# Kernel tuning notes

Measured on AMD Instinct MI355X. Metric: run time of the kernel, lower is better.

Reference implementation:

```python
import jax, jax.numpy as jnp
import numpy as np

N, E, C, NB = 10000, 160000, 32, 8  # atoms, edges, channels, radial basis


def _W(k, shp):
    return jax.random.normal(k, shp, jnp.float32) / np.float32(np.sqrt(shp[0]))


def setup_inputs():
    ks = jax.random.split(jax.random.key(0), 16)
    return {
        "p1": jax.random.normal(ks[0], (N, C), jnp.float32),
        "p3": jax.random.normal(ks[1], (N, 3, C), jnp.float32),
        "r3": jax.random.normal(ks[2], (E, 3), jnp.float32),
        "basis": jax.random.normal(ks[3], (E, NB), jnp.float32),
        "idx_i": jax.random.randint(ks[4], (E,), 0, N, jnp.int32),
        "idx_j": jax.random.randint(ks[5], (E,), 0, N, jnp.int32),
        "pp1_W": _W(ks[6], (C, C)), "pp1_b": jnp.zeros((C,), jnp.float32),
        "pi1_W1": _W(ks[7], (2 * C, C)), "pi1_b1": jnp.zeros((C,), jnp.float32),
        "pi1_W2": _W(ks[8], (C, 3 * C)), "pi1_b2": jnp.zeros((3 * C,), jnp.float32),
        "pi1_W3": _W(ks[9], (3 * C, 3 * C * NB)),
        "ii1_W": _W(ks[10], (C, C)), "ii1_b": jnp.zeros((C,), jnp.float32),
        "pp3_W": _W(ks[11], (C, C)), "pp3_b": jnp.zeros((C,), jnp.float32),
        "pi3_W1": _W(ks[12], (2 * C, C)), "pi3_b1": jnp.zeros((C,), jnp.float32),
        "pi3_W2": _W(ks[13], (C, C)), "pi3_b2": jnp.zeros((C,), jnp.float32),
        "pi3_W3": _W(ks[14], (C, C * NB)),
        "ii3_W": _W(ks[15], (C, C)), "ii3_b": jnp.zeros((C,), jnp.float32),
    }


def _pi_layer(prop, idx_i, idx_j, basis, W1, b1, W2, b2, W3, out_c):
    # gather both endpoints, concat, linear MLP (no activation, no last bias),
    # contract trailing basis axis with per-edge basis functions
    inter = jnp.concatenate([prop[idx_i], prop[idx_j]], axis=-1)  # [E, ..., 2C]
    h = inter @ W1 + b1
    h = h @ W2 + b2
    h = h @ W3                                   # [E, ..., out_c*NB]
    h = h.reshape(h.shape[:-1] + (out_c, NB))
    return jnp.einsum('e...cb,eb->e...c', h, basis)


def _forward(p1, p3, r3, basis, idx_i, idx_j,
             pp1_W, pp1_b, pi1_W1, pi1_b1, pi1_W2, pi1_b2, pi1_W3, ii1_W, ii1_b,
             pp3_W, pp3_b, pi3_W1, pi3_b1, pi3_W2, pi3_b2, pi3_W3, ii3_W, ii3_b):
    act = jnp.tanh
    # rank-1 branch
    p1h = act(p1 @ pp1_W + pp1_b)                                   # [N, C]
    i1 = _pi_layer(p1h, idx_i, idx_j, basis,
                   pi1_W1, pi1_b1, pi1_W2, pi1_b2, pi1_W3, 3 * C)   # [E, 3C]
    i1_1, i1_2, i1_3 = jnp.split(i1, 3, axis=-1)
    i1a = act(i1_1 @ ii1_W + ii1_b)                                  # [E, C]
    p1n = jax.ops.segment_sum(i1a, idx_j, num_segments=N)            # [N, C]
    # rank-3 (vector) branch
    p3h = act(p3 @ pp3_W + pp3_b)                                    # [N, 3, C]
    i3 = _pi_layer(p3h, idx_i, idx_j, basis,
                   pi3_W1, pi3_b1, pi3_W2, pi3_b2, pi3_W3, C)        # [E, 3, C]
    i3 = act(i3 @ ii3_W + ii3_b)
    # equivariant scale/add: i3*i1_2 + r3*i1_3 (broadcast over Cartesian axis)
    i3 = i3 * i1_2[:, None, :] + r3[:, :, None] * i1_3[:, None, :]   # [E, 3, C]
    p3n = jax.ops.segment_sum(i3, idx_j, num_segments=N)             # [N, 3, C]
    # dot layer + residual into p1, then rescale p3 by p1
    p1o = jnp.sum(p3n * p3n, axis=1) + p1n                           # [N, C]
    p3o = p3n * p1o[:, None, :]                                      # [N, 3, C]
    return p1o, p3o


def reference(p1, p3, r3, basis, idx_i, idx_j,
              pp1_W, pp1_b, pi1_W1, pi1_b1, pi1_W2, pi1_b2, pi1_W3, ii1_W, ii1_b,
              pp3_W, pp3_b, pi3_W1, pi3_b1, pi3_W2, pi3_b2, pi3_W3, ii3_W, ii3_b):
    return _forward(p1, p3, r3, basis, idx_i, idx_j,
                    pp1_W, pp1_b, pi1_W1, pi1_b1, pi1_W2, pi1_b2, pi1_W3, ii1_W, ii1_b,
                    pp3_W, pp3_b, pi3_W1, pi3_b1, pi3_W2, pi3_b2, pi3_W3, ii3_W, ii3_b)
```

## Files before the change

kernel.cpp:

```cpp
#include <hip/hip_runtime.h>
#include <math.h>

#define NN 10000
#define NE 160000

typedef __attribute__((ext_vector_type(8))) short s8v;
typedef __attribute__((ext_vector_type(4))) float f4v;
typedef unsigned short u16;

#define OFF_P1HB 0u
#define OFF_P3HB 640000u
#define OFF_WB   2560000u
#define OFF_P1N  2736640u
#define OFF_P3N  4016640u

#define OWF1  0
#define OBB1  49152
#define OII1T 52224
#define OWF3  53248
#define OBB3  69632
#define OII3T 70656
#define NWB   71680

__device__ __forceinline__ short f2b(float f) {
    unsigned u = __float_as_uint(f);
    u += 0x7fffu + ((u >> 16) & 1u);
    return (short)(u >> 16);
}
__device__ __forceinline__ float tanhf_fast(float x) {
    float xc = fminf(9.f, fmaxf(-9.f, x));
    float e = __expf(2.f * xc);
    return (e - 1.f) * __builtin_amdgcn_rcpf(e + 1.f);
}

__global__ __launch_bounds__(256) void prep_kernel(
    const float* __restrict__ p1, const float* __restrict__ p3,
    const float* __restrict__ pp1_W, const float* __restrict__ pp1_b,
    const float* __restrict__ pp3_W, const float* __restrict__ pp3_b,
    const float* __restrict__ W1, const float* __restrict__ W2,
    const float* __restrict__ W3,
    const float* __restrict__ b1v, const float* __restrict__ b2v,
    const float* __restrict__ ii1,
    const float* __restrict__ W13, const float* __restrict__ W23,
    const float* __restrict__ W33,
    const float* __restrict__ b13v, const float* __restrict__ b23v,
    const float* __restrict__ ii3,
    u16* __restrict__ p1hb, u16* __restrict__ p3hb,
    u16* __restrict__ wb, float* __restrict__ p1n)
{
    __shared__ float smem[6912];
    const int blk = blockIdx.x;
    const int tid = threadIdx.x;

    if (blk < 64) {
        const int cb0 = blk * 12;
        float* sW1  = smem;
        float* sW2  = smem + 2048;
        float* sW3c = smem + 5120;
        float* sU   = smem + 6272;
        float* sbt  = smem + 6656;
        for (int i = tid; i < 2048; i += 256) sW1[i] = W1[i];
        for (int i = tid; i < 3072; i += 256) sW2[i] = W2[i];
        for (int i = tid; i < 1152; i += 256) {
            int q = i / 12, u = i % 12;
            sW3c[i] = W3[q * 768 + cb0 + u];
        }
        __syncthreads();
        for (int t = tid; t < 480; t += 256) {
            if (t < 384) {
                int c2 = t / 12, u = t % 12;
                float a = 0.f;
                #pragma unroll 8
                for (int q = 0; q < 96; ++q) a += sW2[c2 * 96 + q] * sW3c[q * 12 + u];
                sU[t] = a;
            } else {
                int q = t - 384;
                float a = b2v[q];
                #pragma unroll 8
                for (int c2 = 0; c2 < 32; ++c2) a += b1v[c2] * sW2[c2 * 96 + q];
                sbt[q] = a;
            }
        }
        __syncthreads();
        for (int o = tid; o < 768; o += 256) {
            int k = o / 12, u = o % 12;
            float a = 0.f;
            #pragma unroll 8
            for (int c2 = 0; c2 < 32; ++c2) a += sW1[k * 32 + c2] * sU[c2 * 12 + u];
            int cb = cb0 + u, b = cb & 7, c = cb >> 3;
            int nt = c >> 4, cL = c & 15;
            int ks = k >> 5, k5 = k & 31, Lhi = k5 >> 3, j = k5 & 7;
            wb[OWF1 + b * 6144 + nt * 1024 + ks * 512 + (Lhi * 16 + cL) * 8 + j] = (u16)f2b(a);
        }
        for (int o = tid; o < 48; o += 256) {
            int u = o >> 2, Lhi = o & 3;
            int x = cb0 + u;
            float a = 0.f;
            if (Lhi == 0) {
                #pragma unroll 8
                for (int q = 0; q < 96; ++q) a += sbt[q] * sW3c[q * 12 + u];
            }
            int j = x & 7, c = x >> 3, nt = c >> 4, cL = c & 15;
            wb[OBB1 + nt * 512 + (Lhi * 16 + cL) * 8 + j] = (u16)f2b(a);
        }
    } else if (blk < 96) {
        const int cb0 = (blk - 64) * 8;
        float* sW13  = smem;
        float* sW23  = smem + 2048;
        float* sW33c = smem + 3072;
        float* sU3   = smem + 3328;
        float* sbt3  = smem + 3584;
        for (int i = tid; i < 2048; i += 256) sW13[i] = W13[i];
        for (int i = tid; i < 1024; i += 256) sW23[i] = W23[i];
        for (int i = tid; i < 256; i += 256) {
            int q = i / 8, u = i % 8;
            sW33c[i] = W33[q * 256 + cb0 + u];
        }
        __syncthreads();
        for (int t = tid; t < 288; t += 256) {
            if (t < 256) {
                int c2 = t / 8, u = t % 8;
                float a = 0.f;
                #pragma unroll 8
                for (int q = 0; q < 32; ++q) a += sW23[c2 * 32 + q] * sW33c[q * 8 + u];
                sU3[t] = a;
            } else {
                int q = t - 256;
                float a = b23v[q];
                #pragma unroll 8
                for (int c2 = 0; c2 < 32; ++c2) a += b13v[c2] * sW23[c2 * 32 + q];
                sbt3[q] = a;
            }
        }
        __syncthreads();
        for (int o = tid; o < 512; o += 256) {
            int k = o / 8, u = o % 8;
            float a = 0.f;
            #pragma unroll 8
            for (int c2 = 0; c2 < 32; ++c2) a += sW13[k * 32 + c2] * sU3[c2 * 8 + u];
            int cb = cb0 + u, b = cb & 7, c = cb >> 3;
            int nt = c >> 4, cL = c & 15;
            int ks = k >> 5, k5 = k & 31, Lhi = k5 >> 3, j = k5 & 7;
            wb[OWF3 + b * 2048 + nt * 1024 + ks * 512 + (Lhi * 16 + cL) * 8 + j] = (u16)f2b(a);
        }
        for (int o = tid; o < 32; o += 256) {
            int u = o >> 2, Lhi = o & 3;
            int x = cb0 + u;
            float a = 0.f;
            if (Lhi == 0) {
                #pragma unroll
                for (int q = 0; q < 32; ++q) a += sbt3[q] * sW33c[q * 8 + u];
            }
            int j = x & 7, c = x >> 3, nt = c >> 4, cL = c & 15;
            wb[OBB3 + nt * 512 + (Lhi * 16 + cL) * 8 + j] = (u16)f2b(a);
        }
    } else if (blk == 96) {
        for (int i = tid; i < 2048; i += 256) {
            if (i < 1024) {
                int nt = i >> 9, L = (i >> 3) & 63, j = i & 7;
                wb[OII1T + i] = (u16)f2b(ii1[((L >> 4) * 8 + j) * 32 + 16 * nt + (L & 15)]);
            } else {
                int i2 = i - 1024;
                int nt = i2 >> 9, L = (i2 >> 3) & 63, j = i2 & 7;
                wb[OII3T + i2] = (u16)f2b(ii3[((L >> 4) * 8 + j) * 32 + 16 * nt + (L & 15)]);
            }
        }
    } else if (blk < 5097) {
        float* Ws0 = smem;
        float* Ws1 = smem + 1024;
        float* bs0 = smem + 2048;
        float* bs1 = smem + 2080;
        for (int i = tid; i < 1024; i += 256) { Ws0[i] = pp1_W[i]; Ws1[i] = pp3_W[i]; }
        if (tid < 32) { bs0[tid] = pp1_b[tid]; bs1[tid] = pp3_b[tid]; }
        __syncthreads();
        int idx = (blk - 97) * 256 + tid;
        int n = idx >> 7;
        int r = (idx >> 5) & 3;
        int c = idx & 31;
        const float* Ws = (r == 0) ? Ws0 : Ws1;
        const float* bs = (r == 0) ? bs0 : bs1;
        const float* in = (r == 0) ? (p1 + n * 32) : (p3 + (n * 3 + (r - 1)) * 32);
        float acc = bs[c];
        #pragma unroll
        for (int k = 0; k < 32; ++k) acc += in[k] * Ws[k * 32 + c];
        short v = f2b(tanhf(acc));
        if (r == 0) p1hb[n * 32 + c] = (u16)v;
        else        p3hb[(n * 3 + (r - 1)) * 32 + c] = (u16)v;
    } else {
        float4 z = make_float4(0.f, 0.f, 0.f, 0.f);
        ((float4*)p1n)[(size_t)(blk - 5097) * 256 + tid] = z;
    }
}

__global__ __launch_bounds__(64, 3) void edge_kernel(
    const u16* __restrict__ p1hb, const u16* __restrict__ p3hb,
    const float* __restrict__ r3, const float* __restrict__ basis,
    const int* __restrict__ idx_i, const int* __restrict__ idx_j,
    const u16* __restrict__ wb,
    const float* __restrict__ ii1b, const float* __restrict__ ii3b,
    float* __restrict__ p1n, float* __restrict__ p3n)
{
    __shared__ int4 smem4[136];
    char* sw = (char*)smem4;
    int*   sIdxI = (int*)(sw + 0);
    int*   sIdxJ = (int*)(sw + 64);
    float* sBasT = (float*)(sw + 128);
    float* sR3   = (float*)(sw + 640);
    u16*   sT2   = (u16*)(sw + 832);

    const int l   = threadIdx.x & 63;
    const int r16 = l & 15;
    const int kg  = l >> 4;
    const int ebase = blockIdx.x * 16;

    if (l < 16)      sIdxI[l] = idx_i[ebase + l];
    else if (l < 32) sIdxJ[l - 16] = idx_j[ebase + l - 16];
    else if (l < 48) {
        int e = l - 32;
        sR3[e]      = r3[(size_t)(ebase + e) * 3 + 0];
        sR3[16 + e] = r3[(size_t)(ebase + e) * 3 + 1];
        sR3[32 + e] = r3[(size_t)(ebase + e) * 3 + 2];
    }
    if (l < 32) {
        int e = l >> 1, hf = l & 1;
        float4 q = ((const float4*)(basis + (size_t)(ebase + e) * 8))[hf];
        sBasT[(4 * hf + 0) * 16 + e] = q.x;
        sBasT[(4 * hf + 1) * 16 + e] = q.y;
        sBasT[(4 * hf + 2) * 16 + e] = q.z;
        sBasT[(4 * hf + 3) * 16 + e] = q.w;
    }

    const float vii1[2] = { ii1b[r16], ii1b[16 + r16] };
    const float vii3[2] = { ii3b[r16], ii3b[16 + r16] };

    const f4v zf = {0.f, 0.f, 0.f, 0.f};

    s8v bA;
    {
        s8v t;
        #pragma unroll
        for (int j = 0; j < 8; ++j)
            t[j] = (kg == 0) ? f2b(sBasT[j * 16 + r16]) : (short)0;
        bA = t;
    }

    s8v avI = *(const s8v*)(p1hb + (size_t)sIdxI[r16] * 32 + kg * 8);
    s8v avJ = *(const s8v*)(p1hb + (size_t)sIdxJ[r16] * 32 + kg * 8);

    f4v accT[6];
    {
        const u16* gBB = wb + OBB1;
        #pragma unroll
        for (int nt = 0; nt < 6; ++nt) {
            s8v bbv = *(const s8v*)(gBB + (nt * 64 + l) * 8);
            accT[nt] = __builtin_amdgcn_mfma_f32_16x16x32_bf16(bA, bbv, zf, 0, 0, 0);
        }
    }

    {
        const u16* gW = wb + OWF1;
        #pragma unroll 2
        for (int b = 0; b < 8; ++b) {
            float tb[4];
            #pragma unroll
            for (int rr = 0; rr < 4; ++rr)
                tb[rr] = sBasT[b * 16 + 4 * kg + rr];
            #pragma unroll
            for (int nt = 0; nt < 6; ++nt) {
                const u16* bp = gW + ((size_t)(b * 6 + nt) * 2) * 512 + l * 8;
                s8v bv0 = *(const s8v*)(bp);
                s8v bv1 = *(const s8v*)(bp + 512);
                f4v D = __builtin_amdgcn_mfma_f32_16x16x32_bf16(avI, bv0, zf, 0, 0, 0);
                D = __builtin_amdgcn_mfma_f32_16x16x32_bf16(avJ, bv1, D, 0, 0, 0);
                #pragma unroll
                for (int rr = 0; rr < 4; ++rr)
                    accT[nt][rr] += tb[rr] * D[rr];
            }
        }
    }

    {
        const u16* gII = wb + OII1T;
        #pragma unroll
        for (int nt = 0; nt < 2; ++nt)
            #pragma unroll
            for (int rr = 0; rr < 4; ++rr)
                sT2[(4 * kg + rr) * 40 + 16 * nt + r16] = (u16)f2b(accT[nt][rr]);
        s8v av = *(const s8v*)(sT2 + r16 * 40 + 8 * kg);
        #pragma unroll
        for (int nt = 0; nt < 2; ++nt) {
            s8v bv = *(const s8v*)(gII + (nt * 64 + l) * 8);
            f4v ia = __builtin_amdgcn_mfma_f32_16x16x32_bf16(av, bv, zf, 0, 0, 0);
            #pragma unroll
            for (int rr = 0; rr < 4; ++rr) {
                int rowD = 4 * kg + rr;
                atomicAdd(&p1n[(size_t)sIdxJ[rowD] * 32 + 16 * nt + r16],
                          tanhf_fast(ia[rr] + vii1[nt]));
            }
        }
    }

    const u16* gW3  = wb + OWF3;
    const u16* gBB3 = wb + OBB3;
    const u16* gII3 = wb + OII3T;
    for (int d = 0; d < 3; ++d) {
        s8v avI3 = *(const s8v*)(p3hb + ((size_t)sIdxI[r16] * 3 + d) * 32 + kg * 8);
        s8v avJ3 = *(const s8v*)(p3hb + ((size_t)sIdxJ[r16] * 3 + d) * 32 + kg * 8);
        f4v accP[2];
        #pragma unroll
        for (int nt = 0; nt < 2; ++nt) {
            s8v bbv = *(const s8v*)(gBB3 + (nt * 64 + l) * 8);
            accP[nt] = __builtin_amdgcn_mfma_f32_16x16x32_bf16(bA, bbv, zf, 0, 0, 0);
        }
        #pragma unroll 2
        for (int b = 0; b < 8; ++b) {
            float tb[4];
            #pragma unroll
            for (int rr = 0; rr < 4; ++rr)
                tb[rr] = sBasT[b * 16 + 4 * kg + rr];
            #pragma unroll
            for (int nt = 0; nt < 2; ++nt) {
                const u16* bp = gW3 + ((size_t)(b * 2 + nt) * 2) * 512 + l * 8;
                s8v bv0 = *(const s8v*)(bp);
                s8v bv1 = *(const s8v*)(bp + 512);
                f4v D = __builtin_amdgcn_mfma_f32_16x16x32_bf16(avI3, bv0, zf, 0, 0, 0);
                D = __builtin_amdgcn_mfma_f32_16x16x32_bf16(avJ3, bv1, D, 0, 0, 0);
                #pragma unroll
                for (int rr = 0; rr < 4; ++rr)
                    accP[nt][rr] += tb[rr] * D[rr];
            }
        }
        #pragma unroll
        for (int nt = 0; nt < 2; ++nt)
            #pragma unroll
            for (int rr = 0; rr < 4; ++rr)
                sT2[(4 * kg + rr) * 40 + 16 * nt + r16] = (u16)f2b(accP[nt][rr]);
        s8v av = *(const s8v*)(sT2 + r16 * 40 + 8 * kg);
        #pragma unroll
        for (int nt = 0; nt < 2; ++nt) {
            s8v bv = *(const s8v*)(gII3 + (nt * 64 + l) * 8);
            f4v ja = __builtin_amdgcn_mfma_f32_16x16x32_bf16(av, bv, zf, 0, 0, 0);
            #pragma unroll
            for (int rr = 0; rr < 4; ++rr) {
                int rowD = 4 * kg + rr;
                float i3a = tanhf_fast(ja[rr] + vii3[nt]);
                float val = i3a * accT[2 + nt][rr] + sR3[d * 16 + rowD] * accT[4 + nt][rr];
                atomicAdd(&p3n[((size_t)sIdxJ[rowD] * 3 + d) * 32 + 16 * nt + r16], val);
            }
        }
    }
}

__global__ __launch_bounds__(256) void finalize_kernel(
    const float* __restrict__ p1n, const float* __restrict__ p3n,
    float* __restrict__ out)
{
    int t = blockIdx.x * 256 + threadIdx.x;
    int n = t >> 5, c = t & 31;
    float a0 = p3n[(n * 3 + 0) * 32 + c];
    float a1 = p3n[(n * 3 + 1) * 32 + c];
    float a2 = p3n[(n * 3 + 2) * 32 + c];
    float p1o = p1n[t] + a0 * a0 + a1 * a1 + a2 * a2;
    out[t] = p1o;
    float* o3 = out + NN * 32;
    o3[(n * 3 + 0) * 32 + c] = a0 * p1o;
    o3[(n * 3 + 1) * 32 + c] = a1 * p1o;
    o3[(n * 3 + 2) * 32 + c] = a2 * p1o;
}

extern "C" void kernel_launch(void* const* d_in, const int* in_sizes, int n_in,
                              void* d_out, int out_size, void* d_ws, size_t ws_size,
                              hipStream_t stream) {
    const float* p1     = (const float*)d_in[0];
    const float* p3     = (const float*)d_in[1];
    const float* r3     = (const float*)d_in[2];
    const float* basis  = (const float*)d_in[3];
    const int*   idx_i  = (const int*)d_in[4];
    const int*   idx_j  = (const int*)d_in[5];
    const float* pp1_W  = (const float*)d_in[6];
    const float* pp1_b  = (const float*)d_in[7];
    const float* pi1_W1 = (const float*)d_in[8];
    const float* pi1_b1 = (const float*)d_in[9];
    const float* pi1_W2 = (const float*)d_in[10];
    const float* pi1_b2 = (const float*)d_in[11];
    const float* pi1_W3 = (const float*)d_in[12];
    const float* ii1_W  = (const float*)d_in[13];
    const float* ii1_b  = (const float*)d_in[14];
    const float* pp3_W  = (const float*)d_in[15];
    const float* pp3_b  = (const float*)d_in[16];
    const float* pi3_W1 = (const float*)d_in[17];
    const float* pi3_b1 = (const float*)d_in[18];
    const float* pi3_W2 = (const float*)d_in[19];
    const float* pi3_b2 = (const float*)d_in[20];
    const float* pi3_W3 = (const float*)d_in[21];
    const float* ii3_W  = (const float*)d_in[22];
    const float* ii3_b  = (const float*)d_in[23];

    char* ws = (char*)d_ws;
    u16*   p1hb = (u16*)(ws + OFF_P1HB);
    u16*   p3hb = (u16*)(ws + OFF_P3HB);
    u16*   wb   = (u16*)(ws + OFF_WB);
    float* p1n  = (float*)(ws + OFF_P1N);
    float* p3n  = (float*)(ws + OFF_P3N);

    prep_kernel<<<dim3(6347), dim3(256), 0, stream>>>(
        p1, p3, pp1_W, pp1_b, pp3_W, pp3_b,
        pi1_W1, pi1_W2, pi1_W3, pi1_b1, pi1_b2, ii1_W,
        pi3_W1, pi3_W2, pi3_W3, pi3_b1, pi3_b2, ii3_W,
        p1hb, p3hb, wb, p1n);

    edge_kernel<<<dim3(NE / 16), dim3(64), 0, stream>>>(
        p1hb, p3hb, r3, basis, idx_i, idx_j, wb,
        ii1_b, ii3_b, p1n, p3n);

    finalize_kernel<<<dim3(1250), dim3(256), 0, stream>>>(p1n, p3n, (float*)d_out);
}
```

Before: 125.4 us.

## Replace atomic scatter with counting-sort ranks and per-node gather reduction

```diff
diff --git a/kernel.cpp b/kernel.cpp
--- a/kernel.cpp
+++ b/kernel.cpp
@@ -8,11 +8,14 @@
 typedef __attribute__((ext_vector_type(4))) float f4v;
 typedef unsigned short u16;
 
-#define OFF_P1HB 0u
-#define OFF_P3HB 640000u
-#define OFF_WB   2560000u
-#define OFF_P1N  2736640u
-#define OFF_P3N  4016640u
+#define OFF_P1HB  0u
+#define OFF_P3HB  640000u
+#define OFF_WB    2560000u
+#define OFF_HIST  2703360u
+#define OFF_CURSOR 2743360u
+#define OFF_START 2783360u
+#define OFF_RANK  2823364u
+#define OFF_E13   3463376u
 
 #define OWF1  0
 #define OBB1  49152
@@ -26,6 +29,9 @@
     unsigned u = __float_as_uint(f);
     u += 0x7fffu + ((u >> 16) & 1u);
     return (short)(u >> 16);
+}
+__device__ __forceinline__ float b2f(u16 s) {
+    return __uint_as_float(((unsigned)s) << 16);
 }
 __device__ __forceinline__ float tanhf_fast(float x) {
     float xc = fminf(9.f, fmaxf(-9.f, x));
@@ -45,8 +51,9 @@
     const float* __restrict__ W33,
     const float* __restrict__ b13v, const float* __restrict__ b23v,
     const float* __restrict__ ii3,
+    const int* __restrict__ idx_j,
     u16* __restrict__ p1hb, u16* __restrict__ p3hb,
-    u16* __restrict__ wb, float* __restrict__ p1n)
+    u16* __restrict__ wb, int* __restrict__ hist)
 {
     __shared__ float smem[6912];
     const int blk = blockIdx.x;
@@ -187,18 +194,52 @@
         if (r == 0) p1hb[n * 32 + c] = (u16)v;
         else        p3hb[(n * 3 + (r - 1)) * 32 + c] = (u16)v;
     } else {
-        float4 z = make_float4(0.f, 0.f, 0.f, 0.f);
-        ((float4*)p1n)[(size_t)(blk - 5097) * 256 + tid] = z;
-    }
+        int e = (blk - 5097) * 256 + tid;
+        if (e < NE) atomicAdd(&hist[idx_j[e]], 1);
+    }
+}
+
+__global__ __launch_bounds__(256) void scan_kernel(
+    const int* __restrict__ hist, int* __restrict__ start, int* __restrict__ cursor)
+{
+    __shared__ int part[256];
+    int t = threadIdx.x;
+    int base = t * 40;
+    int s = 0;
+    for (int i = 0; i < 40; ++i) { int idx = base + i; if (idx < NN) s += hist[idx]; }
+    part[t] = s;
+    __syncthreads();
+    for (int off = 1; off < 256; off <<= 1) {
+        int v = (t >= off) ? part[t - off] : 0;
+        __syncthreads();
+        part[t] += v;
+        __syncthreads();
+    }
+    int run = part[t] - s;
+    for (int i = 0; i < 40; ++i) {
+        int idx = base + i;
+        if (idx < NN) {
+            int h = hist[idx];
+            start[idx] = run; cursor[idx] = run; run += h;
+        }
+    }
+    if (t == 255) start[NN] = part[255];
+}
+
+__global__ __launch_bounds__(256) void rank_kernel(
+    const int* __restrict__ idx_j, int* __restrict__ cursor, int* __restrict__ rank)
+{
+    int e = blockIdx.x * 256 + threadIdx.x;
+    if (e < NE) rank[e] = atomicAdd(&cursor[idx_j[e]], 1);
 }
 
 __global__ __launch_bounds__(64, 3) void edge_kernel(
     const u16* __restrict__ p1hb, const u16* __restrict__ p3hb,
     const float* __restrict__ r3, const float* __restrict__ basis,
     const int* __restrict__ idx_i, const int* __restrict__ idx_j,
-    const u16* __restrict__ wb,
+    const int* __restrict__ rank, const u16* __restrict__ wb,
     const float* __restrict__ ii1b, const float* __restrict__ ii3b,
-    float* __restrict__ p1n, float* __restrict__ p3n)
+    u16* __restrict__ e13)
 {
     __shared__ int4 smem4[136];
     char* sw = (char*)smem4;
@@ -206,7 +247,8 @@
     int*   sIdxJ = (int*)(sw + 64);
     float* sBasT = (float*)(sw + 128);
     float* sR3   = (float*)(sw + 640);
-    u16*   sT2   = (u16*)(sw + 832);
+    int*   sRank = (int*)(sw + 832);
+    u16*   sT2   = (u16*)(sw + 896);
 
     const int l   = threadIdx.x & 63;
     const int r16 = l & 15;
@@ -220,6 +262,8 @@
         sR3[e]      = r3[(size_t)(ebase + e) * 3 + 0];
         sR3[16 + e] = r3[(size_t)(ebase + e) * 3 + 1];
         sR3[32 + e] = r3[(size_t)(ebase + e) * 3 + 2];
+    } else {
+        sRank[l - 48] = rank[ebase + l - 48];
     }
     if (l < 32) {
         int e = l >> 1, hf = l & 1;
@@ -287,16 +331,16 @@
             for (int rr = 0; rr < 4; ++rr)
                 sT2[(4 * kg + rr) * 40 + 16 * nt + r16] = (u16)f2b(accT[nt][rr]);
         s8v av = *(const s8v*)(sT2 + r16 * 40 + 8 * kg);
-        #pragma unroll
-        for (int nt = 0; nt < 2; ++nt) {
-            s8v bv = *(const s8v*)(gII + (nt * 64 + l) * 8);
-            f4v ia = __builtin_amdgcn_mfma_f32_16x16x32_bf16(av, bv, zf, 0, 0, 0);
-            #pragma unroll
-            for (int rr = 0; rr < 4; ++rr) {
-                int rowD = 4 * kg + rr;
-                atomicAdd(&p1n[(size_t)sIdxJ[rowD] * 32 + 16 * nt + r16],
-                          tanhf_fast(ia[rr] + vii1[nt]));
-            }
+        s8v bvA = *(const s8v*)(gII + (0 * 64 + l) * 8);
+        s8v bvB = *(const s8v*)(gII + (1 * 64 + l) * 8);
+        f4v ia0 = __builtin_amdgcn_mfma_f32_16x16x32_bf16(av, bvA, zf, 0, 0, 0);
+        f4v ia1 = __builtin_amdgcn_mfma_f32_16x16x32_bf16(av, bvB, zf, 0, 0, 0);
+        #pragma unroll
+        for (int rr = 0; rr < 4; ++rr) {
+            int rowD = 4 * kg + rr;
+            size_t base = (size_t)sRank[rowD] * 128;
+            e13[base + r16]      = (u16)f2b(tanhf_fast(ia0[rr] + vii1[0]));
+            e13[base + 16 + r16] = (u16)f2b(tanhf_fast(ia1[rr] + vii1[1]));
         }
     }
 
@@ -336,36 +380,62 @@
             for (int rr = 0; rr < 4; ++rr)
                 sT2[(4 * kg + rr) * 40 + 16 * nt + r16] = (u16)f2b(accP[nt][rr]);
         s8v av = *(const s8v*)(sT2 + r16 * 40 + 8 * kg);
-        #pragma unroll
-        for (int nt = 0; nt < 2; ++nt) {
-            s8v bv = *(const s8v*)(gII3 + (nt * 64 + l) * 8);
-            f4v ja = __builtin_amdgcn_mfma_f32_16x16x32_bf16(av, bv, zf, 0, 0, 0);
-            #pragma unroll
-            for (int rr = 0; rr < 4; ++rr) {
-                int rowD = 4 * kg + rr;
-                float i3a = tanhf_fast(ja[rr] + vii3[nt]);
-                float val = i3a * accT[2 + nt][rr] + sR3[d * 16 + rowD] * accT[4 + nt][rr];
-                atomicAdd(&p3n[((size_t)sIdxJ[rowD] * 3 + d) * 32 + 16 * nt + r16], val);
-            }
-        }
-    }
-}
-
-__global__ __launch_bounds__(256) void finalize_kernel(
-    const float* __restrict__ p1n, const float* __restrict__ p3n,
+        s8v bvA = *(const s8v*)(gII3 + (0 * 64 + l) * 8);
+        s8v bvB = *(const s8v*)(gII3 + (1 * 64 + l) * 8);
+        f4v ja0 = __builtin_amdgcn_mfma_f32_16x16x32_bf16(av, bvA, zf, 0, 0, 0);
+        f4v ja1 = __builtin_amdgcn_mfma_f32_16x16x32_bf16(av, bvB, zf, 0, 0, 0);
+        #pragma unroll
+        for (int rr = 0; rr < 4; ++rr) {
+            int rowD = 4 * kg + rr;
+            float rv = sR3[d * 16 + rowD];
+            float v0 = tanhf_fast(ja0[rr] + vii3[0]) * accT[2][rr] + rv * accT[4][rr];
+            float v1 = tanhf_fast(ja1[rr] + vii3[1]) * accT[3][rr] + rv * accT[5][rr];
+            size_t base = (size_t)sRank[rowD] * 128 + 32 + 32 * d;
+            e13[base + r16]      = (u16)f2b(v0);
+            e13[base + 16 + r16] = (u16)f2b(v1);
+        }
+    }
+}
+
+__global__ __launch_bounds__(256) void gather2(
+    const u16* __restrict__ e13, const int* __restrict__ start,
     float* __restrict__ out)
 {
-    int t = blockIdx.x * 256 + threadIdx.x;
-    int n = t >> 5, c = t & 31;
-    float a0 = p3n[(n * 3 + 0) * 32 + c];
-    float a1 = p3n[(n * 3 + 1) * 32 + c];
-    float a2 = p3n[(n * 3 + 2) * 32 + c];
-    float p1o = p1n[t] + a0 * a0 + a1 * a1 + a2 * a2;
-    out[t] = p1o;
-    float* o3 = out + NN * 32;
-    o3[(n * 3 + 0) * 32 + c] = a0 * p1o;
-    o3[(n * 3 + 1) * 32 + c] = a1 * p1o;
-    o3[(n * 3 + 2) * 32 + c] = a2 * p1o;
+    int node = blockIdx.x * 4 + (threadIdx.x >> 6);
+    int l = threadIdx.x & 63;
+    int st = start[node], en = start[node + 1];
+    int deg = en - st;
+    float a0 = 0.f, a1 = 0.f;
+    const u16* base = e13 + (size_t)st * 128 + 2 * l;
+    int k = 0;
+    for (; k + 4 <= deg; k += 4) {
+        unsigned v0 = *(const unsigned*)(base + (size_t)(k + 0) * 128);
+        unsigned v1 = *(const unsigned*)(base + (size_t)(k + 1) * 128);
+        unsigned v2 = *(const unsigned*)(base + (size_t)(k + 2) * 128);
+        unsigned v3 = *(const unsigned*)(base + (size_t)(k + 3) * 128);
+        a0 += b2f((u16)(v0 & 0xffffu)) + b2f((u16)(v1 & 0xffffu))
+            + b2f((u16)(v2 & 0xffffu)) + b2f((u16)(v3 & 0xffffu));
+        a1 += b2f((u16)(v0 >> 16)) + b2f((u16)(v1 >> 16))
+            + b2f((u16)(v2 >> 16)) + b2f((u16)(v3 >> 16));
+    }
+    for (; k < deg; ++k) {
+        unsigned v = *(const unsigned*)(base + (size_t)k * 128);
+        a0 += b2f((u16)(v & 0xffffu));
+        a1 += b2f((u16)(v >> 16));
+    }
+    int q = l & 15, g = l >> 4;
+    float s00 = __shfl(a0, q),      s10 = __shfl(a1, q);
+    float s01 = __shfl(a0, 16 + q), s11 = __shfl(a1, 16 + q);
+    float s02 = __shfl(a0, 32 + q), s12 = __shfl(a1, 32 + q);
+    float s03 = __shfl(a0, 48 + q), s13 = __shfl(a1, 48 + q);
+    float p1o0 = s00 + s01 * s01 + s02 * s02 + s03 * s03;
+    float p1o1 = s10 + s11 * s11 + s12 * s12 + s13 * s13;
+    if (g == 0) {
+        *(float2*)(out + (size_t)node * 32 + 2 * q) = make_float2(p1o0, p1o1);
+    } else {
+        float2 v = make_float2(a0 * p1o0, a1 * p1o1);
+        *(float2*)(out + (size_t)NN * 32 + ((size_t)node * 3 + (g - 1)) * 32 + 2 * q) = v;
+    }
 }
 
 extern "C" void kernel_launch(void* const* d_in, const int* in_sizes, int n_in,
@@ -397,21 +467,29 @@
     const float* ii3_b  = (const float*)d_in[23];
 
     char* ws = (char*)d_ws;
-    u16*   p1hb = (u16*)(ws + OFF_P1HB);
-    u16*   p3hb = (u16*)(ws + OFF_P3HB);
-    u16*   wb   = (u16*)(ws + OFF_WB);
-    float* p1n  = (float*)(ws + OFF_P1N);
-    float* p3n  = (float*)(ws + OFF_P3N);
-
-    prep_kernel<<<dim3(6347), dim3(256), 0, stream>>>(
+    u16* p1hb   = (u16*)(ws + OFF_P1HB);
+    u16* p3hb   = (u16*)(ws + OFF_P3HB);
+    u16* wb     = (u16*)(ws + OFF_WB);
+    int* hist   = (int*)(ws + OFF_HIST);
+    int* cursor = (int*)(ws + OFF_CURSOR);
+    int* startA = (int*)(ws + OFF_START);
+    int* rank   = (int*)(ws + OFF_RANK);
+    u16* e13    = (u16*)(ws + OFF_E13);
+
+    hipMemsetAsync(hist, 0, NN * sizeof(int), stream);
+
+    prep_kernel<<<dim3(5722), dim3(256), 0, stream>>>(
         p1, p3, pp1_W, pp1_b, pp3_W, pp3_b,
         pi1_W1, pi1_W2, pi1_W3, pi1_b1, pi1_b2, ii1_W,
         pi3_W1, pi3_W2, pi3_W3, pi3_b1, pi3_b2, ii3_W,
-        p1hb, p3hb, wb, p1n);
+        idx_j, p1hb, p3hb, wb, hist);
+
+    scan_kernel<<<dim3(1), dim3(256), 0, stream>>>(hist, startA, cursor);
+    rank_kernel<<<dim3((NE + 255) / 256), dim3(256), 0, stream>>>(idx_j, cursor, rank);
 
     edge_kernel<<<dim3(NE / 16), dim3(64), 0, stream>>>(
-        p1hb, p3hb, r3, basis, idx_i, idx_j, wb,
-        ii1_b, ii3_b, p1n, p3n);
-
-    finalize_kernel<<<dim3(1250), dim3(256), 0, stream>>>(p1n, p3n, (float*)d_out);
-}
+        p1hb, p3hb, r3, basis, idx_i, idx_j, rank, wb,
+        ii1_b, ii3_b, e13);
+
+    gather2<<<dim3(2500), dim3(256), 0, stream>>>(e13, startA, (float*)d_out);
+}
```

Result: slower. 162.3 us (+29.5%).
